# Performance work log

Hardware: AMD Instinct MI355X
Metric: run time of the kernel (lower is better)

Reference implementation:

```python
import jax, jax.numpy as jnp
import numpy as np

FEAT = 36          # 4 + node_embedding_dim(32)
N_NODES = 24       # max_num_nodes_per_route
N_ROUTES = 48      # max_num_route
CUST_H = 128
CUST_OUT = 32
RNN_H = 128        # route_output_dim
B = 512


def _xavier(key, shape):
    fan_in, fan_out = shape[0], shape[1]
    lim = float(np.sqrt(6.0 / (fan_in + fan_out)))
    return jax.random.uniform(key, shape, jnp.float32, -lim, lim)


def setup_inputs() -> dict:
    key = jax.random.key(0)
    ks = jax.random.split(key, 24)
    inp = {
        "candidates": jax.random.normal(ks[0], (B, 2 * FEAT), jnp.float32),
        "customers": jax.random.normal(ks[1], (B, N_ROUTES, N_NODES * FEAT), jnp.float32),
        # Customer_Model MLP: 36 -> 128 (tanh) -> 32 (tanh)
        "cust_w1": _xavier(ks[2], (FEAT, CUST_H)),
        "cust_b1": jnp.zeros((CUST_H,), jnp.float32),
        "cust_w2": _xavier(ks[3], (CUST_H, CUST_OUT)),
        "cust_b2": jnp.zeros((CUST_OUT,), jnp.float32),
        # GRU layer 0 (input 32 -> hidden 128), gates order (r,z,n)
        "gru_wih0": _xavier(ks[4], (CUST_OUT, 3 * RNN_H)),
        "gru_whh0": _xavier(ks[5], (RNN_H, 3 * RNN_H)),
        "gru_bih0": jnp.zeros((3 * RNN_H,), jnp.float32),
        "gru_bhh0": jnp.zeros((3 * RNN_H,), jnp.float32),
        # GRU layer 1 (128 -> 128)
        "gru_wih1": _xavier(ks[6], (RNN_H, 3 * RNN_H)),
        "gru_whh1": _xavier(ks[7], (RNN_H, 3 * RNN_H)),
        "gru_bih1": jnp.zeros((3 * RNN_H,), jnp.float32),
        "gru_bhh1": jnp.zeros((3 * RNN_H,), jnp.float32),
        # candidate head and final MLP
        "cand_w": _xavier(ks[8], (2 * FEAT, 64)),
        "cand_b": jnp.zeros((64,), jnp.float32),
        "fc1_w": _xavier(ks[9], (RNN_H + 64, 128)),
        "fc1_b": jnp.zeros((128,), jnp.float32),
        "fc2_w": _xavier(ks[10], (128, 128)),
        "fc2_b": jnp.zeros((128,), jnp.float32),
        "fc3_w": _xavier(ks[11], (128, 1)),
        "fc3_b": jnp.zeros((1,), jnp.float32),
    }
    return inp


def _gru_layer(x_seq, wih, whh, bih, bhh):
    # x_seq: [T, N, in_dim]; returns [T, N, RNN_H]
    gi = jnp.einsum('tni,ih->tnh', x_seq, wih) + bih  # precompute input gates

    def step(h, gi_t):
        gh = h @ whh + bhh
        i_r, i_z, i_n = jnp.split(gi_t, 3, axis=-1)
        h_r, h_z, h_n = jnp.split(gh, 3, axis=-1)
        r = jax.nn.sigmoid(i_r + h_r)
        z = jax.nn.sigmoid(i_z + h_z)
        n = jnp.tanh(i_n + r * h_n)
        h_new = (1.0 - z) * n + z * h
        return h_new, h_new

    h0 = jnp.zeros((x_seq.shape[1], RNN_H), x_seq.dtype)
    _, out = jax.lax.scan(step, h0, gi)
    return out


def reference(candidates, customers, cust_w1, cust_b1, cust_w2, cust_b2,
              gru_wih0, gru_whh0, gru_bih0, gru_bhh0,
              gru_wih1, gru_whh1, gru_bih1, gru_bhh1,
              cand_w, cand_b, fc1_w, fc1_b, fc2_w, fc2_b, fc3_w, fc3_b):
    b = candidates.shape[0]
    x_c = candidates @ cand_w + cand_b                      # [B, 64]

    # all routes processed at once: fold routes into batch dim
    x = customers.reshape(b * N_ROUTES, N_NODES, FEAT)
    x = jnp.transpose(x, (1, 0, 2))                          # [T=24, B*48, 36]
    # Customer_Model MLP (tanh hidden, tanh output)
    x = jnp.tanh(jnp.tanh(x @ cust_w1 + cust_b1) @ cust_w2 + cust_b2)  # [24, B*48, 32]

    out = _gru_layer(x, gru_wih0, gru_whh0, gru_bih0, gru_bhh0)
    out = _gru_layer(out, gru_wih1, gru_whh1, gru_bih1, gru_bhh1)
    last = out[-1].reshape(b, N_ROUTES, RNN_H)               # last timestep per route
    x_r = last.mean(axis=1)                                  # mean over 48 routes
    # dropout is identity at inference

    h = jnp.concatenate([x_r, x_c], axis=1)                  # [B, 192]
    h = jnp.tanh(h @ fc1_w + fc1_b)
    h = jnp.tanh(h @ fc2_w + fc2_b)
    return h @ fc3_w + fc3_b                                 # [B, 1]
```

## Files before the change

### kernel.cpp

```cpp
#include <hip/hip_runtime.h>
#include <stdint.h>


#define NSEQ   24576
#define TSTEPS 24

typedef __attribute__((ext_vector_type(8))) short bf16x8;
typedef __attribute__((ext_vector_type(4))) float floatx4;

#define PK_W1    0
#define PK_W2    8192
#define PK_WIH0  12288
#define PK_WHH0  24576
#define PK_WIH1  73728
#define PK_WHH1  122880
#define PK_END   172032
#define X2_EL    172032
#define HOUT_BYTE 38092800

#define MFMA(a,b,c) c = __builtin_amdgcn_mfma_f32_16x16x32_bf16(a, b, c, 0, 0, 0)

__device__ __forceinline__ uint16_t f2bf(float f) {
  uint32_t u = __float_as_uint(f);
  u += 0x7FFFu + ((u >> 16) & 1u);
  return (uint16_t)(u >> 16);
}
__device__ __forceinline__ uint32_t cvt_pk(float a, float b) {
  uint32_t r;
  asm("v_cvt_pk_bf16_f32 %0, %1, %2" : "=v"(r) : "v"(a), "v"(b));
  return r;
}
__device__ __forceinline__ float fast_sigmoid(float x) {
  float e = __builtin_amdgcn_exp2f(-1.4426950408889634f * x);
  return __builtin_amdgcn_rcpf(1.0f + e);
}
__device__ __forceinline__ float fast_tanh(float x) {
  float e = __builtin_amdgcn_exp2f(-2.8853900817779268f * x);
  return 2.0f * __builtin_amdgcn_rcpf(1.0f + e) - 1.0f;
}
__device__ __forceinline__ bf16x8 ldf(const uint16_t* p) {
  return *(const bf16x8*)p;
}

__global__ __launch_bounds__(256) void pack_weights(
    const float* __restrict__ w1, const float* __restrict__ w2,
    const float* __restrict__ wih0, const float* __restrict__ whh0,
    const float* __restrict__ wih1, const float* __restrict__ whh1,
    uint16_t* __restrict__ ws) {
  int idx = blockIdx.x * 256 + threadIdx.x;
  if (idx >= PK_END) return;
  const float* W; int N, KB, Kreal, base;
  if      (idx <  8192) { W = w1;   N = 128; KB = 2; Kreal = 36;  base = 0; }
  else if (idx < 12288) { W = w2;   N = 32;  KB = 4; Kreal = 128; base = 8192; }
  else if (idx < 24576) { W = wih0; N = 384; KB = 1; Kreal = 32;  base = 12288; }
  else if (idx < 73728) { W = whh0; N = 384; KB = 4; Kreal = 128; base = 24576; }
  else if (idx < 122880){ W = wih1; N = 384; KB = 4; Kreal = 128; base = 73728; }
  else                  { W = whh1; N = 384; KB = 4; Kreal = 128; base = 122880; }
  int li = idx - base;
  int frag = li >> 9;
  int e = li & 511;
  int lane = e >> 3, j = e & 7;
  int kb = frag % KB, nt = frag / KB;
  int k = kb * 32 + (lane >> 4) * 8 + j;
  int n = nt * 16 + (lane & 15);
  float v = (k < Kreal) ? W[k * N + n] : 0.0f;
  ws[base + li] = f2bf(v);
}

__global__ __launch_bounds__(256) void mlp_kernel(
    const float* __restrict__ customers, const float* __restrict__ b1,
    const float* __restrict__ b2, const uint16_t* __restrict__ wpk,
    uint16_t* __restrict__ x2out) {
  __shared__ uint16_t sA[128 * 136];
  const int r0 = blockIdx.x * 128;
  const int t  = r0 / NSEQ;
  const int s0 = r0 % NSEQ;
  const int tid = threadIdx.x;
  const int w = tid >> 6, l = tid & 63, q = l >> 4, c = l & 15;
  const int lo8 = l * 8;
  const int hb = 4 * q;

  floatx4 acc[2][8];
  #pragma unroll
  for (int mi = 0; mi < 2; ++mi)
    #pragma unroll
    for (int nt = 0; nt < 8; ++nt) acc[mi][nt] = (floatx4){0.f, 0.f, 0.f, 0.f};

  #pragma unroll
  for (int mi = 0; mi < 2; ++mi) {
    const int mt = 2 * w + mi;
    const int seq = s0 + mt * 16 + c;
    const float* xp = customers + (size_t)seq * 864 + t * 36;
    floatx4 u0 = *(const floatx4*)(xp + q * 8);
    floatx4 u1 = *(const floatx4*)(xp + q * 8 + 4);
    bf16x8 a0;
    { uint32_t* a0u = (uint32_t*)&a0;
      a0u[0] = cvt_pk(u0[0], u0[1]); a0u[1] = cvt_pk(u0[2], u0[3]);
      a0u[2] = cvt_pk(u1[0], u1[1]); a0u[3] = cvt_pk(u1[2], u1[3]); }
    bf16x8 a1x = (bf16x8){0,0,0,0,0,0,0,0};
    if (q == 0) {
      floatx4 u2 = *(const floatx4*)(xp + 32);
      uint32_t* a1u = (uint32_t*)&a1x;
      a1u[0] = cvt_pk(u2[0], u2[1]); a1u[1] = cvt_pk(u2[2], u2[3]);
    }
    #pragma unroll
    for (int nt = 0; nt < 8; ++nt) {
      bf16x8 bv0 = ldf(wpk + PK_W1 + (nt * 2 + 0) * 512 + lo8);
      bf16x8 bv1 = ldf(wpk + PK_W1 + (nt * 2 + 1) * 512 + lo8);
      MFMA(bv0, a0,  acc[mi][nt]);
      MFMA(bv1, a1x, acc[mi][nt]);
    }
  }
  #pragma unroll
  for (int mi = 0; mi < 2; ++mi) {
    const int mt = 2 * w + mi;
    #pragma unroll
    for (int nt = 0; nt < 8; ++nt) {
      const floatx4 bv = *(const floatx4*)(b1 + nt * 16 + hb);
      float o0 = fast_tanh(acc[mi][nt][0] + bv[0]);
      float o1 = fast_tanh(acc[mi][nt][1] + bv[1]);
      float o2 = fast_tanh(acc[mi][nt][2] + bv[2]);
      float o3 = fast_tanh(acc[mi][nt][3] + bv[3]);
      uint2 pk; pk.x = cvt_pk(o0, o1); pk.y = cvt_pk(o2, o3);
      *(uint2*)&sA[(mt * 16 + c) * 136 + nt * 16 + hb] = pk;
    }
  }
  __syncthreads();

  floatx4 acc2[2][2];
  #pragma unroll
  for (int mi = 0; mi < 2; ++mi)
    #pragma unroll
    for (int nt = 0; nt < 2; ++nt) acc2[mi][nt] = (floatx4){0.f, 0.f, 0.f, 0.f};

  #pragma unroll
  for (int kb = 0; kb < 4; ++kb) {
    bf16x8 av0 = ldf(&sA[((2 * w + 0) * 16 + c) * 136 + kb * 32 + q * 8]);
    bf16x8 av1 = ldf(&sA[((2 * w + 1) * 16 + c) * 136 + kb * 32 + q * 8]);
    #pragma unroll
    for (int nt = 0; nt < 2; ++nt) {
      bf16x8 bv = ldf(wpk + PK_W2 + (nt * 4 + kb) * 512 + lo8);
      MFMA(bv, av0, acc2[0][nt]);
      MFMA(bv, av1, acc2[1][nt]);
    }
  }
  #pragma unroll
  for (int mi = 0; mi < 2; ++mi) {
    const int mt = 2 * w + mi;
    #pragma unroll
    for (int nt = 0; nt < 2; ++nt) {
      const floatx4 bv = *(const floatx4*)(b2 + nt * 16 + hb);
      float o0 = fast_tanh(acc2[mi][nt][0] + bv[0]);
      float o1 = fast_tanh(acc2[mi][nt][1] + bv[1]);
      float o2 = fast_tanh(acc2[mi][nt][2] + bv[2]);
      float o3 = fast_tanh(acc2[mi][nt][3] + bv[3]);
      uint2 pk; pk.x = cvt_pk(o0, o1); pk.y = cvt_pk(o2, o3);
      *(uint2*)(x2out + (size_t)(r0 + mt * 16 + c) * 32 + nt * 16 + hb) = pk;
    }
  }
}

__global__ __launch_bounds__(512, 2) void gru_res(
    const uint16_t* __restrict__ wpk, const uint16_t* __restrict__ x2,
    const float* __restrict__ bih0, const float* __restrict__ bhh0,
    const float* __restrict__ bih1, const float* __restrict__ bhh1,
    float* __restrict__ hout) {
  __shared__ uint16_t hl[2][2][32 * 136];
  const int seq0 = blockIdx.x * 32;
  const int tid = threadIdx.x;
  const int J = tid >> 6, l = tid & 63, q = l >> 4, c = l & 15;
  const int lo8 = l * 8;

  { uint32_t* z = (uint32_t*)hl;
    for (int i = tid; i < 8704; i += 512) z[i] = 0u; }

  bf16x8 wi0[3], wh0[3][4], wi1[3][4], wh1[3][4];
  #pragma unroll
  for (int g = 0; g < 3; ++g) {
    wi0[g] = ldf(wpk + PK_WIH0 + (g * 8 + J) * 512 + lo8);
    #pragma unroll
    for (int kb = 0; kb < 4; ++kb) {
      wh0[g][kb] = ldf(wpk + PK_WHH0 + ((g * 8 + J) * 4 + kb) * 512 + lo8);
      wi1[g][kb] = ldf(wpk + PK_WIH1 + ((g * 8 + J) * 4 + kb) * 512 + lo8);
      wh1[g][kb] = ldf(wpk + PK_WHH1 + ((g * 8 + J) * 4 + kb) * 512 + lo8);
    }
  }
  const int hb = J * 16 + 4 * q;
  const floatx4 vR0 = *(const floatx4*)(bih0 + hb)       + *(const floatx4*)(bhh0 + hb);
  const floatx4 vZ0 = *(const floatx4*)(bih0 + 128 + hb) + *(const floatx4*)(bhh0 + 128 + hb);
  const floatx4 vN0 = *(const floatx4*)(bih0 + 256 + hb);
  const floatx4 vH0 = *(const floatx4*)(bhh0 + 256 + hb);
  const floatx4 vR1 = *(const floatx4*)(bih1 + hb)       + *(const floatx4*)(bhh1 + hb);
  const floatx4 vZ1 = *(const floatx4*)(bih1 + 128 + hb) + *(const floatx4*)(bhh1 + 128 + hb);
  const floatx4 vN1 = *(const floatx4*)(bih1 + 256 + hb);
  const floatx4 vH1 = *(const floatx4*)(bhh1 + 256 + hb);

  floatx4 h0m[2], h1m[2];
  h0m[0] = (floatx4){0.f, 0.f, 0.f, 0.f}; h0m[1] = (floatx4){0.f, 0.f, 0.f, 0.f};
  h1m[0] = (floatx4){0.f, 0.f, 0.f, 0.f}; h1m[1] = (floatx4){0.f, 0.f, 0.f, 0.f};

  bf16x8 axc[2];
  axc[0] = ldf(x2 + (size_t)(seq0 + c) * 32 + q * 8);
  axc[1] = ldf(x2 + (size_t)(seq0 + 16 + c) * 32 + q * 8);
  __syncthreads();

  #pragma unroll 1
  for (int t = 0; t < TSTEPS; ++t) {
    const int cur = t & 1, prv = cur ^ 1;
    const int tn = (t < TSTEPS - 1) ? t + 1 : t;
    bf16x8 axn0 = ldf(x2 + ((size_t)tn * NSEQ + seq0 + c) * 32 + q * 8);
    bf16x8 axn1 = ldf(x2 + ((size_t)tn * NSEQ + seq0 + 16 + c) * 32 + q * 8);

    uint16_t* h0w = hl[0][cur]; const uint16_t* h0r = hl[0][prv];
    uint16_t* h1w = hl[1][cur]; const uint16_t* h1r = hl[1][prv];

    {
      floatx4 aR[2], aZ[2], aN[2], aH[2];
      #pragma unroll
      for (int mi = 0; mi < 2; ++mi) {
        aR[mi] = vR0; aZ[mi] = vZ0; aN[mi] = vN0; aH[mi] = vH0;
      }
      #pragma unroll
      for (int kb = 0; kb < 4; ++kb) {
        bf16x8 a0 = ldf(h0r + (c)      * 136 + kb * 32 + q * 8);
        bf16x8 a1 = ldf(h0r + (16 + c) * 136 + kb * 32 + q * 8);
        MFMA(wh0[0][kb], a0, aR[0]); MFMA(wh0[0][kb], a1, aR[1]);
        MFMA(wh0[1][kb], a0, aZ[0]); MFMA(wh0[1][kb], a1, aZ[1]);
        MFMA(wh0[2][kb], a0, aH[0]); MFMA(wh0[2][kb], a1, aH[1]);
      }
      MFMA(wi0[0], axc[0], aR[0]); MFMA(wi0[0], axc[1], aR[1]);
      MFMA(wi0[1], axc[0], aZ[0]); MFMA(wi0[1], axc[1], aZ[1]);
      MFMA(wi0[2], axc[0], aN[0]); MFMA(wi0[2], axc[1], aN[1]);
      #pragma unroll
      for (int mi = 0; mi < 2; ++mi) {
        float o[4];
        #pragma unroll
        for (int e = 0; e < 4; ++e) {
          float r  = fast_sigmoid(aR[mi][e]);
          float zz = fast_sigmoid(aZ[mi][e]);
          float nn = fast_tanh(aN[mi][e] + r * aH[mi][e]);
          o[e] = nn + zz * (h0m[mi][e] - nn);
          h0m[mi][e] = o[e];
        }
        uint2 pk; pk.x = cvt_pk(o[0], o[1]); pk.y = cvt_pk(o[2], o[3]);
        *(uint2*)(h0w + (mi * 16 + c) * 136 + hb) = pk;
      }
    }
    __syncthreads();

    {
      floatx4 aR[2], aZ[2], aN[2], aH[2];
      #pragma unroll
      for (int mi = 0; mi < 2; ++mi) {
        aR[mi] = vR1; aZ[mi] = vZ1; aN[mi] = vN1; aH[mi] = vH1;
      }
      #pragma unroll
      for (int kb = 0; kb < 4; ++kb) {
        bf16x8 ai0 = ldf(h0w + (c)      * 136 + kb * 32 + q * 8);
        bf16x8 ai1 = ldf(h0w + (16 + c) * 136 + kb * 32 + q * 8);
        bf16x8 ah0 = ldf(h1r + (c)      * 136 + kb * 32 + q * 8);
        bf16x8 ah1 = ldf(h1r + (16 + c) * 136 + kb * 32 + q * 8);
        MFMA(wi1[0][kb], ai0, aR[0]); MFMA(wi1[0][kb], ai1, aR[1]);
        MFMA(wi1[1][kb], ai0, aZ[0]); MFMA(wi1[1][kb], ai1, aZ[1]);
        MFMA(wi1[2][kb], ai0, aN[0]); MFMA(wi1[2][kb], ai1, aN[1]);
        MFMA(wh1[0][kb], ah0, aR[0]); MFMA(wh1[0][kb], ah1, aR[1]);
        MFMA(wh1[1][kb], ah0, aZ[0]); MFMA(wh1[1][kb], ah1, aZ[1]);
        MFMA(wh1[2][kb], ah0, aH[0]); MFMA(wh1[2][kb], ah1, aH[1]);
      }
      #pragma unroll
      for (int mi = 0; mi < 2; ++mi) {
        float o[4];
        #pragma unroll
        for (int e = 0; e < 4; ++e) {
          float r  = fast_sigmoid(aR[mi][e]);
          float zz = fast_sigmoid(aZ[mi][e]);
          float nn = fast_tanh(aN[mi][e] + r * aH[mi][e]);
          o[e] = nn + zz * (h1m[mi][e] - nn);
          h1m[mi][e] = o[e];
        }
        uint2 pk; pk.x = cvt_pk(o[0], o[1]); pk.y = cvt_pk(o[2], o[3]);
        *(uint2*)(h1w + (mi * 16 + c) * 136 + hb) = pk;
      }
    }
    __syncthreads();
    axc[0] = axn0; axc[1] = axn1;
  }

  #pragma unroll
  for (int mi = 0; mi < 2; ++mi)
    *(floatx4*)(hout + (size_t)(seq0 + mi * 16 + c) * 128 + hb) = h1m[mi];
}

__global__ __launch_bounds__(192) void final_kernel(
    const float* __restrict__ hout, const float* __restrict__ cands,
    const float* __restrict__ cw, const float* __restrict__ cb,
    const float* __restrict__ f1w, const float* __restrict__ f1b,
    const float* __restrict__ f2w, const float* __restrict__ f2b,
    const float* __restrict__ f3w, const float* __restrict__ f3b,
    float* __restrict__ out) {
  __shared__ float hc[192];
  __shared__ float v1[128];
  __shared__ float v2[128];
  __shared__ float red[128];
  const int b = blockIdx.x, tid = threadIdx.x;
  if (tid < 128) {
    float s = 0.f;
    const float* hp = hout + (size_t)(b * 48) * 128 + tid;
    #pragma unroll 4
    for (int r = 0; r < 48; ++r) s += hp[r * 128];
    hc[tid] = s * (1.0f / 48.0f);
  } else {
    int j = tid - 128;
    float s = cb[j];
    const float* cp = cands + b * 72;
    #pragma unroll 8
    for (int k = 0; k < 72; ++k) s += cp[k] * cw[k * 64 + j];
    hc[128 + j] = s;
  }
  __syncthreads();
  if (tid < 128) {
    float s = f1b[tid];
    for (int k = 0; k < 192; ++k) s += hc[k] * f1w[k * 128 + tid];
    v1[tid] = fast_tanh(s);
  }
  __syncthreads();
  if (tid < 128) {
    float s = f2b[tid];
    for (int k = 0; k < 128; ++k) s += v1[k] * f2w[k * 128 + tid];
    v2[tid] = fast_tanh(s);
  }
  __syncthreads();
  if (tid < 128) red[tid] = v2[tid] * f3w[tid];
  __syncthreads();
  if (tid < 64) {
    float s = red[tid] + red[tid + 64];
    s += __shfl_down(s, 32);
    s += __shfl_down(s, 16);
    s += __shfl_down(s, 8);
    s += __shfl_down(s, 4);
    s += __shfl_down(s, 2);
    s += __shfl_down(s, 1);
    if (tid == 0) out[b] = s + f3b[0];
  }
}

extern "C" void kernel_launch(void* const* d_in, const int* in_sizes, int n_in,
                              void* d_out, int out_size, void* d_ws, size_t ws_size,
                              hipStream_t stream) {
  const float* cand  = (const float*)d_in[0];
  const float* cust  = (const float*)d_in[1];
  const float* w1    = (const float*)d_in[2];
  const float* b1    = (const float*)d_in[3];
  const float* w2    = (const float*)d_in[4];
  const float* b2    = (const float*)d_in[5];
  const float* wih0  = (const float*)d_in[6];
  const float* whh0  = (const float*)d_in[7];
  const float* bih0  = (const float*)d_in[8];
  const float* bhh0  = (const float*)d_in[9];
  const float* wih1  = (const float*)d_in[10];
  const float* whh1  = (const float*)d_in[11];
  const float* bih1  = (const float*)d_in[12];
  const float* bhh1  = (const float*)d_in[13];
  const float* cw    = (const float*)d_in[14];
  const float* cb    = (const float*)d_in[15];
  const float* f1w   = (const float*)d_in[16];
  const float* f1b   = (const float*)d_in[17];
  const float* f2w   = (const float*)d_in[18];
  const float* f2b   = (const float*)d_in[19];
  const float* f3w   = (const float*)d_in[20];
  const float* f3b   = (const float*)d_in[21];

  uint16_t* wsp = (uint16_t*)d_ws;
  uint16_t* x2p = wsp + X2_EL;
  float* hout = (float*)((char*)d_ws + HOUT_BYTE);
  float* outp = (float*)d_out;

  pack_weights<<<(PK_END + 255) / 256, 256, 0, stream>>>(w1, w2, wih0, whh0, wih1, whh1, wsp);
  mlp_kernel<<<(NSEQ * TSTEPS) / 128, 256, 0, stream>>>(cust, b1, b2, wsp, x2p);
  gru_res<<<NSEQ / 32, 512, 0, stream>>>(wsp, x2p, bih0, bhh0, bih1, bhh1, hout);
  final_kernel<<<512, 192, 0, stream>>>(hout, cand, cw, cb, f1w, f1b, f2w, f2b, f3w, f3b, outp);
}
```

Before: 440.2 us.

## Skew the two GRU layers so each step needs one barrier, and halve sequences per block

```diff
diff --git a/kernel.cpp b/kernel.cpp
--- a/kernel.cpp
+++ b/kernel.cpp
@@ -4,6 +4,7 @@
 
 #define NSEQ   24576
 #define TSTEPS 24
+#define SEQB   16
 
 typedef __attribute__((ext_vector_type(8))) short bf16x8;
 typedef __attribute__((ext_vector_type(4))) float floatx4;
@@ -165,14 +166,28 @@
     const float* __restrict__ bih0, const float* __restrict__ bhh0,
     const float* __restrict__ bih1, const float* __restrict__ bhh1,
     float* __restrict__ hout) {
-  __shared__ uint16_t hl[2][2][32 * 136];
-  const int seq0 = blockIdx.x * 32;
+  __shared__ uint16_t h0l[2][SEQB * 136];
+  __shared__ uint16_t h1l[2][SEQB * 136];
+  __shared__ float bias_l[8][128];
+  const int seq0 = blockIdx.x * SEQB;
   const int tid = threadIdx.x;
   const int J = tid >> 6, l = tid & 63, q = l >> 4, c = l & 15;
   const int lo8 = l * 8;
 
-  { uint32_t* z = (uint32_t*)hl;
-    for (int i = tid; i < 8704; i += 512) z[i] = 0u; }
+  for (int i = tid; i < 1088; i += 512) ((uint32_t*)h1l[0])[i] = 0u;
+  for (int i = tid; i < 1024; i += 512) {
+    int g = i >> 7, k = i & 127;
+    float v;
+    if      (g == 0) v = bih0[k]       + bhh0[k];
+    else if (g == 1) v = bih0[128 + k] + bhh0[128 + k];
+    else if (g == 2) v = bih0[256 + k];
+    else if (g == 3) v = bhh0[256 + k];
+    else if (g == 4) v = bih1[k]       + bhh1[k];
+    else if (g == 5) v = bih1[128 + k] + bhh1[128 + k];
+    else if (g == 6) v = bih1[256 + k];
+    else             v = bhh1[256 + k];
+    bias_l[g][k] = v;
+  }
 
   bf16x8 wi0[3], wh0[3][4], wi1[3][4], wh1[3][4];
   #pragma unroll
@@ -186,109 +201,95 @@
     }
   }
   const int hb = J * 16 + 4 * q;
-  const floatx4 vR0 = *(const floatx4*)(bih0 + hb)       + *(const floatx4*)(bhh0 + hb);
-  const floatx4 vZ0 = *(const floatx4*)(bih0 + 128 + hb) + *(const floatx4*)(bhh0 + 128 + hb);
-  const floatx4 vN0 = *(const floatx4*)(bih0 + 256 + hb);
-  const floatx4 vH0 = *(const floatx4*)(bhh0 + 256 + hb);
-  const floatx4 vR1 = *(const floatx4*)(bih1 + hb)       + *(const floatx4*)(bhh1 + hb);
-  const floatx4 vZ1 = *(const floatx4*)(bih1 + 128 + hb) + *(const floatx4*)(bhh1 + 128 + hb);
-  const floatx4 vN1 = *(const floatx4*)(bih1 + 256 + hb);
-  const floatx4 vH1 = *(const floatx4*)(bhh1 + 256 + hb);
-
-  floatx4 h0m[2], h1m[2];
-  h0m[0] = (floatx4){0.f, 0.f, 0.f, 0.f}; h0m[1] = (floatx4){0.f, 0.f, 0.f, 0.f};
-  h1m[0] = (floatx4){0.f, 0.f, 0.f, 0.f}; h1m[1] = (floatx4){0.f, 0.f, 0.f, 0.f};
-
-  bf16x8 axc[2];
-  axc[0] = ldf(x2 + (size_t)(seq0 + c) * 32 + q * 8);
-  axc[1] = ldf(x2 + (size_t)(seq0 + 16 + c) * 32 + q * 8);
+
+  floatx4 h0m, h1m = (floatx4){0.f, 0.f, 0.f, 0.f};
+
+  bf16x8 ax0 = ldf(x2 + (size_t)(seq0 + c) * 32 + q * 8);
+  bf16x8 ax  = ldf(x2 + ((size_t)NSEQ + seq0 + c) * 32 + q * 8);
+  __syncthreads();
+
+  {
+    floatx4 aR = *(const floatx4*)&bias_l[0][hb];
+    floatx4 aZ = *(const floatx4*)&bias_l[1][hb];
+    floatx4 aN = *(const floatx4*)&bias_l[2][hb];
+    floatx4 aH = *(const floatx4*)&bias_l[3][hb];
+    MFMA(wi0[0], ax0, aR); MFMA(wi0[1], ax0, aZ); MFMA(wi0[2], ax0, aN);
+    float o[4];
+    #pragma unroll
+    for (int e = 0; e < 4; ++e) {
+      float r  = fast_sigmoid(aR[e]);
+      float zz = fast_sigmoid(aZ[e]);
+      float nn = fast_tanh(aN[e] + r * aH[e]);
+      o[e] = nn - zz * nn;
+      h0m[e] = o[e];
+    }
+    uint2 pk; pk.x = cvt_pk(o[0], o[1]); pk.y = cvt_pk(o[2], o[3]);
+    *(uint2*)(h0l[0] + c * 136 + hb) = pk;
+  }
   __syncthreads();
 
   #pragma unroll 1
   for (int t = 0; t < TSTEPS; ++t) {
-    const int cur = t & 1, prv = cur ^ 1;
-    const int tn = (t < TSTEPS - 1) ? t + 1 : t;
-    bf16x8 axn0 = ldf(x2 + ((size_t)tn * NSEQ + seq0 + c) * 32 + q * 8);
-    bf16x8 axn1 = ldf(x2 + ((size_t)tn * NSEQ + seq0 + 16 + c) * 32 + q * 8);
-
-    uint16_t* h0w = hl[0][cur]; const uint16_t* h0r = hl[0][prv];
-    uint16_t* h1w = hl[1][cur]; const uint16_t* h1r = hl[1][prv];
+    const uint16_t* h0cur = h0l[t & 1];
+    const uint16_t* h1prv = h1l[t & 1];
+    uint16_t* h0nxt = h0l[(t + 1) & 1];
+    uint16_t* h1cur = h1l[(t + 1) & 1];
+    const int tnx = (t + 2 < TSTEPS) ? t + 2 : TSTEPS - 1;
+    bf16x8 axn = ldf(x2 + ((size_t)tnx * NSEQ + seq0 + c) * 32 + q * 8);
+
+    floatx4 aR1 = *(const floatx4*)&bias_l[4][hb];
+    floatx4 aZ1 = *(const floatx4*)&bias_l[5][hb];
+    floatx4 aN1 = *(const floatx4*)&bias_l[6][hb];
+    floatx4 aH1 = *(const floatx4*)&bias_l[7][hb];
+    floatx4 aR0 = *(const floatx4*)&bias_l[0][hb];
+    floatx4 aZ0 = *(const floatx4*)&bias_l[1][hb];
+    floatx4 aN0 = *(const floatx4*)&bias_l[2][hb];
+    floatx4 aH0 = *(const floatx4*)&bias_l[3][hb];
+
+    #pragma unroll
+    for (int kb = 0; kb < 4; ++kb) {
+      bf16x8 a0 = ldf(h0cur + c * 136 + kb * 32 + q * 8);
+      bf16x8 ah = ldf(h1prv + c * 136 + kb * 32 + q * 8);
+      MFMA(wi1[0][kb], a0, aR1); MFMA(wh1[0][kb], ah, aR1);
+      MFMA(wi1[1][kb], a0, aZ1); MFMA(wh1[1][kb], ah, aZ1);
+      MFMA(wi1[2][kb], a0, aN1); MFMA(wh1[2][kb], ah, aH1);
+      MFMA(wh0[0][kb], a0, aR0);
+      MFMA(wh0[1][kb], a0, aZ0);
+      MFMA(wh0[2][kb], a0, aH0);
+    }
+    MFMA(wi0[0], ax, aR0); MFMA(wi0[1], ax, aZ0); MFMA(wi0[2], ax, aN0);
 
     {
-      floatx4 aR[2], aZ[2], aN[2], aH[2];
+      float o[4];
       #pragma unroll
-      for (int mi = 0; mi < 2; ++mi) {
-        aR[mi] = vR0; aZ[mi] = vZ0; aN[mi] = vN0; aH[mi] = vH0;
+      for (int e = 0; e < 4; ++e) {
+        float r  = fast_sigmoid(aR1[e]);
+        float zz = fast_sigmoid(aZ1[e]);
+        float nn = fast_tanh(aN1[e] + r * aH1[e]);
+        o[e] = nn + zz * (h1m[e] - nn);
+        h1m[e] = o[e];
       }
+      uint2 pk; pk.x = cvt_pk(o[0], o[1]); pk.y = cvt_pk(o[2], o[3]);
+      *(uint2*)(h1cur + c * 136 + hb) = pk;
+    }
+    {
+      float o[4];
       #pragma unroll
-      for (int kb = 0; kb < 4; ++kb) {
-        bf16x8 a0 = ldf(h0r + (c)      * 136 + kb * 32 + q * 8);
-        bf16x8 a1 = ldf(h0r + (16 + c) * 136 + kb * 32 + q * 8);
-        MFMA(wh0[0][kb], a0, aR[0]); MFMA(wh0[0][kb], a1, aR[1]);
-        MFMA(wh0[1][kb], a0, aZ[0]); MFMA(wh0[1][kb], a1, aZ[1]);
-        MFMA(wh0[2][kb], a0, aH[0]); MFMA(wh0[2][kb], a1, aH[1]);
+      for (int e = 0; e < 4; ++e) {
+        float r  = fast_sigmoid(aR0[e]);
+        float zz = fast_sigmoid(aZ0[e]);
+        float nn = fast_tanh(aN0[e] + r * aH0[e]);
+        o[e] = nn + zz * (h0m[e] - nn);
+        h0m[e] = o[e];
       }
-      MFMA(wi0[0], axc[0], aR[0]); MFMA(wi0[0], axc[1], aR[1]);
-      MFMA(wi0[1], axc[0], aZ[0]); MFMA(wi0[1], axc[1], aZ[1]);
-      MFMA(wi0[2], axc[0], aN[0]); MFMA(wi0[2], axc[1], aN[1]);
-      #pragma unroll
-      for (int mi = 0; mi < 2; ++mi) {
-        float o[4];
-        #pragma unroll
-        for (int e = 0; e < 4; ++e) {
-          float r  = fast_sigmoid(aR[mi][e]);
-          float zz = fast_sigmoid(aZ[mi][e]);
-          float nn = fast_tanh(aN[mi][e] + r * aH[mi][e]);
-          o[e] = nn + zz * (h0m[mi][e] - nn);
-          h0m[mi][e] = o[e];
-        }
-        uint2 pk; pk.x = cvt_pk(o[0], o[1]); pk.y = cvt_pk(o[2], o[3]);
-        *(uint2*)(h0w + (mi * 16 + c) * 136 + hb) = pk;
-      }
+      uint2 pk; pk.x = cvt_pk(o[0], o[1]); pk.y = cvt_pk(o[2], o[3]);
+      *(uint2*)(h0nxt + c * 136 + hb) = pk;
     }
     __syncthreads();
-
-    {
-      floatx4 aR[2], aZ[2], aN[2], aH[2];
-      #pragma unroll
-      for (int mi = 0; mi < 2; ++mi) {
-        aR[mi] = vR1; aZ[mi] = vZ1; aN[mi] = vN1; aH[mi] = vH1;
-      }
-      #pragma unroll
-      for (int kb = 0; kb < 4; ++kb) {
-        bf16x8 ai0 = ldf(h0w + (c)      * 136 + kb * 32 + q * 8);
-        bf16x8 ai1 = ldf(h0w + (16 + c) * 136 + kb * 32 + q * 8);
-        bf16x8 ah0 = ldf(h1r + (c)      * 136 + kb * 32 + q * 8);
-        bf16x8 ah1 = ldf(h1r + (16 + c) * 136 + kb * 32 + q * 8);
-        MFMA(wi1[0][kb], ai0, aR[0]); MFMA(wi1[0][kb], ai1, aR[1]);
-        MFMA(wi1[1][kb], ai0, aZ[0]); MFMA(wi1[1][kb], ai1, aZ[1]);
-        MFMA(wi1[2][kb], ai0, aN[0]); MFMA(wi1[2][kb], ai1, aN[1]);
-        MFMA(wh1[0][kb], ah0, aR[0]); MFMA(wh1[0][kb], ah1, aR[1]);
-        MFMA(wh1[1][kb], ah0, aZ[0]); MFMA(wh1[1][kb], ah1, aZ[1]);
-        MFMA(wh1[2][kb], ah0, aH[0]); MFMA(wh1[2][kb], ah1, aH[1]);
-      }
-      #pragma unroll
-      for (int mi = 0; mi < 2; ++mi) {
-        float o[4];
-        #pragma unroll
-        for (int e = 0; e < 4; ++e) {
-          float r  = fast_sigmoid(aR[mi][e]);
-          float zz = fast_sigmoid(aZ[mi][e]);
-          float nn = fast_tanh(aN[mi][e] + r * aH[mi][e]);
-          o[e] = nn + zz * (h1m[mi][e] - nn);
-          h1m[mi][e] = o[e];
-        }
-        uint2 pk; pk.x = cvt_pk(o[0], o[1]); pk.y = cvt_pk(o[2], o[3]);
-        *(uint2*)(h1w + (mi * 16 + c) * 136 + hb) = pk;
-      }
-    }
-    __syncthreads();
-    axc[0] = axn0; axc[1] = axn1;
-  }
-
-  #pragma unroll
-  for (int mi = 0; mi < 2; ++mi)
-    *(floatx4*)(hout + (size_t)(seq0 + mi * 16 + c) * 128 + hb) = h1m[mi];
+    ax = axn;
+  }
+
+  *(floatx4*)(hout + (size_t)(seq0 + c) * 128 + hb) = h1m;
 }
 
 __global__ __launch_bounds__(192) void final_kernel(
@@ -377,6 +378,6 @@
 
   pack_weights<<<(PK_END + 255) / 256, 256, 0, stream>>>(w1, w2, wih0, whh0, wih1, whh1, wsp);
   mlp_kernel<<<(NSEQ * TSTEPS) / 128, 256, 0, stream>>>(cust, b1, b2, wsp, x2p);
-  gru_res<<<NSEQ / 32, 512, 0, stream>>>(wsp, x2p, bih0, bhh0, bih1, bhh1, hout);
+  gru_res<<<NSEQ / SEQB, 512, 0, stream>>>(wsp, x2p, bih0, bhh0, bih1, bhh1, hout);
   final_kernel<<<512, 192, 0, stream>>>(hout, cand, cw, cb, f1w, f1b, f2w, f2b, f3w, f3b, outp);
 }
```

Measured after the change: 420.0 us. 4.6% less time.
